# Optimization experiments

Hardware: AMD Instinct MI355X
Metric: run time of the kernel (lower is better)

Reference implementation:

```python
import jax, jax.numpy as jnp
import numpy as np

B, C, H, W = 16, 64, 64, 64
K = 512  # n_embeddings


def setup_inputs() -> dict:
    key = jax.random.key(0)
    k1, k2 = jax.random.split(key)
    inputs = jax.random.normal(k1, (B, C, H, W), dtype=jnp.float32)
    emb_weight = jax.random.normal(k2, (K, C), dtype=jnp.float32)
    weight = jnp.ones((K,), dtype=jnp.float32)  # EMA cluster-size buffer
    return {"inputs": inputs, "emb_weight": emb_weight, "weight": weight}


def reference(inputs, emb_weight, weight):
    sg = jax.lax.stop_gradient
    # BCHW -> BHWC
    x = jnp.transpose(inputs, (0, 2, 3, 1))  # [B,H,W,C]
    flat = x.reshape(-1, x.shape[-1])        # [N,C]
    n = flat.shape[0]
    k = emb_weight.shape[0]
    # squared euclidean distances [N,K] (argmin identical to cdist argmin)
    d = (
        jnp.sum(flat * flat, axis=-1, keepdims=True)
        - 2.0 * (flat @ emb_weight.T)
        + jnp.sum(emb_weight * emb_weight, axis=-1)
    )
    indices = jnp.argmin(d, axis=1)  # [N]
    # avg_probs = mean over rows of one-hot mask == normalized histogram
    avg_probs = jnp.bincount(indices, length=k).astype(jnp.float32) / jnp.float32(n)
    perplexity = jnp.exp(-jnp.sum(avg_probs * jnp.log(avg_probs + 1e-10)))
    # straight-through quantization
    q = emb_weight[indices].reshape(x.shape)  # [B,H,W,C]
    quantized = sg(q) + x - sg(x)
    commitment_loss = jnp.mean((sg(quantized) - x) ** 2)
    active_codes = jnp.sum(weight >= 0.01)
    out = jnp.transpose(quantized, (0, 3, 1, 2))  # back to BCHW
    return out, commitment_loss, perplexity, active_codes, indices
```

## Files before the change

kernel.cpp:

```cpp
#include <hip/hip_runtime.h>

#define HW 4096
#define CHW 262144
#define OUT_ELEMS 4194304
#define FLT_BIG 3.4e38f

typedef __attribute__((ext_vector_type(8))) short  short8;
typedef __attribute__((ext_vector_type(4))) float  floatx4;
typedef __attribute__((ext_vector_type(4))) int    intx4;


__device__ __forceinline__ unsigned bf16_rne(float f) {
    unsigned u = __float_as_uint(f);
    return (u + 0x7FFFu + ((u >> 16) & 1u)) >> 16;
}

__device__ __forceinline__ void split8(const float* f, intx4* hi, intx4* lo) {
    unsigned h[4], l[4];
#pragma unroll
    for (int j = 0; j < 4; ++j) {
        const unsigned h0 = bf16_rne(f[2 * j]);
        const unsigned h1 = bf16_rne(f[2 * j + 1]);
        const float hf0 = __uint_as_float(h0 << 16);
        const float hf1 = __uint_as_float(h1 << 16);
        const unsigned l0 = bf16_rne(f[2 * j] - hf0);
        const unsigned l1 = bf16_rne(f[2 * j + 1] - hf1);
        h[j] = h0 | (h1 << 16);
        l[j] = l0 | (l1 << 16);
    }
    *hi = intx4{(int)h[0], (int)h[1], (int)h[2], (int)h[3]};
    *lo = intx4{(int)l[0], (int)l[1], (int)l[2], (int)l[3]};
}

__global__ void vq_prep(const float* __restrict__ emb,
                        unsigned short* __restrict__ pfrag,
                        float* __restrict__ enorm) {
    const int t = threadIdx.x;
    const int lane = t & 63;
    const int code = (blockIdx.x << 2) + (t >> 6);
    const int c = lane;
    const float v = emb[(code << 6) + c];
    const unsigned hb = bf16_rne(v);
    const float hf    = __uint_as_float(hb << 16);
    const unsigned lb = bf16_rne(v - hf);
    const int nc = code >> 6, grp = (code & 63) >> 4, n = code & 15;
    const int q = (c & 31) >> 3, o = c & 7;
    const int jh = c >> 5;
    const int jl = 2 + (c >> 5);
    pfrag[((((size_t)(nc*4 + jh)*4 + grp)*4 + q)*16 + n)*8 + o] = (unsigned short)hb;
    pfrag[((((size_t)(nc*4 + jl)*4 + grp)*4 + q)*16 + n)*8 + o] = (unsigned short)lb;
    float s = v * v;
#pragma unroll
    for (int off = 32; off > 0; off >>= 1) s += __shfl_xor(s, off, 64);
    if (lane == 0) enorm[code] = -0.5f * s;
}

__global__ __launch_bounds__(256)
void vq_main(const float* __restrict__ x_in, const float* __restrict__ emb,
             const unsigned short* __restrict__ pfrag,
             const float* __restrict__ enorm,
             float* __restrict__ out, float* __restrict__ idx_out,
             double* __restrict__ ws_sse) {
    __shared__ float  b1s[2][64], b2s[2][64];
    __shared__ int    i1s[2][64], i2s[2][64];
    __shared__ int    c1i[64], c2i[64];
    __shared__ double parts[4][65];
    __shared__ double ls_red[4];

    const int t     = threadIdx.x;
    const int lane  = t & 63;
    const int wv    = t >> 6;
    const int col   = lane & 15;
    const int quad  = lane >> 4;
    const int blk   = blockIdx.x;
    const int khalf = wv & 1;
    const int mset  = wv >> 1;
    const int ncol0 = khalf << 5;
    const int b = blk >> 6, h = blk & 63;
    const float* xb = x_in + (size_t)b * CHW + h * 64;

    short8 Xh[2][2], Xl[2][2];
#pragma unroll
    for (int T = 0; T < 2; ++T) {
        const int row = (mset << 5) + (T << 4) + col;
#pragma unroll
        for (int u = 0; u < 2; ++u) {
            float f[8];
#pragma unroll
            for (int j = 0; j < 8; ++j) {
                const int c = (u << 5) + (quad << 3) + j;
                f[j] = xb[(size_t)c * HW + row];
            }
            intx4 hi, lo;
            split8(f, &hi, &lo);
            Xh[T][u] = __builtin_bit_cast(short8, hi);
            Xl[T][u] = __builtin_bit_cast(short8, lo);
        }
    }

    float B1a[2], B2a[2], B1b[2], B2b[2];
    int   I1a[2], I2a[2], I1b[2], I2b[2];
#pragma unroll
    for (int T = 0; T < 2; ++T) {
        B1a[T] = -FLT_BIG; B2a[T] = -FLT_BIG; B1b[T] = -FLT_BIG; B2b[T] = -FLT_BIG;
        I1a[T] = 0x3FFFFFFF; I2a[T] = 0x3FFFFFFF; I1b[T] = 0x3FFFFFFF; I2b[T] = 0x3FFFFFFF;
    }

    const char*  pf  = (const char*)pfrag + (size_t)lane * 16 + ((size_t)khalf << 11);
    const float* enp = enorm + ncol0 + (quad << 2);

#pragma unroll 2
    for (int nc = 0; nc < 8; ++nc) {
        const char* base = pf + ((size_t)nc << 14);
        const int K0 = nc << 6;
        const floatx4 e0v = *(const floatx4*)(enp + K0);
        const floatx4 e1v = *(const floatx4*)(enp + K0 + 16);
        floatx4 a0[2] = {{0.f,0.f,0.f,0.f},{0.f,0.f,0.f,0.f}};
        floatx4 a1[2] = {{0.f,0.f,0.f,0.f},{0.f,0.f,0.f,0.f}};
#define BLD(j, g) (*(const short8*)(base + ((j) << 12) + ((g) << 10)))
        {
            const short8 e0 = BLD(0, 0), e1 = BLD(0, 1);
#pragma unroll
            for (int T = 0; T < 2; ++T) {
                a0[T] = __builtin_amdgcn_mfma_f32_16x16x32_bf16(e0, Xh[T][0], a0[T], 0, 0, 0);
                a1[T] = __builtin_amdgcn_mfma_f32_16x16x32_bf16(e1, Xh[T][0], a1[T], 0, 0, 0);
                a0[T] = __builtin_amdgcn_mfma_f32_16x16x32_bf16(e0, Xl[T][0], a0[T], 0, 0, 0);
                a1[T] = __builtin_amdgcn_mfma_f32_16x16x32_bf16(e1, Xl[T][0], a1[T], 0, 0, 0);
            }
        }
        {
            const short8 e0 = BLD(1, 0), e1 = BLD(1, 1);
#pragma unroll
            for (int T = 0; T < 2; ++T) {
                a0[T] = __builtin_amdgcn_mfma_f32_16x16x32_bf16(e0, Xh[T][1], a0[T], 0, 0, 0);
                a1[T] = __builtin_amdgcn_mfma_f32_16x16x32_bf16(e1, Xh[T][1], a1[T], 0, 0, 0);
                a0[T] = __builtin_amdgcn_mfma_f32_16x16x32_bf16(e0, Xl[T][1], a0[T], 0, 0, 0);
                a1[T] = __builtin_amdgcn_mfma_f32_16x16x32_bf16(e1, Xl[T][1], a1[T], 0, 0, 0);
            }
        }
        {
            const short8 e0 = BLD(2, 0), e1 = BLD(2, 1);
#pragma unroll
            for (int T = 0; T < 2; ++T) {
                a0[T] = __builtin_amdgcn_mfma_f32_16x16x32_bf16(e0, Xh[T][0], a0[T], 0, 0, 0);
                a1[T] = __builtin_amdgcn_mfma_f32_16x16x32_bf16(e1, Xh[T][0], a1[T], 0, 0, 0);
            }
        }
        {
            const short8 e0 = BLD(3, 0), e1 = BLD(3, 1);
#pragma unroll
            for (int T = 0; T < 2; ++T) {
                a0[T] = __builtin_amdgcn_mfma_f32_16x16x32_bf16(e0, Xh[T][1], a0[T], 0, 0, 0);
                a1[T] = __builtin_amdgcn_mfma_f32_16x16x32_bf16(e1, Xh[T][1], a1[T], 0, 0, 0);
            }
        }
#undef BLD

        const int cb = K0 + ncol0 + (quad << 2);
#pragma unroll
        for (int T = 0; T < 2; ++T) {
#pragma unroll
            for (int reg = 0; reg < 4; ++reg) {
                const float da = a0[T][reg] + e0v[reg];
                if (da > B1a[T])      { B2a[T] = B1a[T]; I2a[T] = I1a[T]; B1a[T] = da; I1a[T] = cb + reg; }
                else if (da > B2a[T]) { B2a[T] = da; I2a[T] = cb + reg; }
                const float db = a1[T][reg] + e1v[reg];
                if (db > B1b[T])      { B2b[T] = B1b[T]; I2b[T] = I1b[T]; B1b[T] = db; I1b[T] = cb + 16 + reg; }
                else if (db > B2b[T]) { B2b[T] = db; I2b[T] = cb + 16 + reg; }
            }
        }
    }

#pragma unroll
    for (int T = 0; T < 2; ++T) {
        float B1, B2; int I1, I2;
        if (B1b[T] > B1a[T] || (B1b[T] == B1a[T] && I1b[T] < I1a[T])) {
            B1 = B1b[T]; I1 = I1b[T];
            if (B1a[T] > B2b[T] || (B1a[T] == B2b[T] && I1a[T] < I2b[T])) { B2 = B1a[T]; I2 = I1a[T]; }
            else                                                          { B2 = B2b[T]; I2 = I2b[T]; }
        } else {
            B1 = B1a[T]; I1 = I1a[T];
            if (B1b[T] > B2a[T] || (B1b[T] == B2a[T] && I1b[T] < I2a[T])) { B2 = B1b[T]; I2 = I1b[T]; }
            else                                                          { B2 = B2a[T]; I2 = I2a[T]; }
        }
#pragma unroll
        for (int off = 16; off <= 32; off <<= 1) {
            const float ob1 = __shfl_xor(B1, off, 64);
            const int   oi1 = __shfl_xor(I1, off, 64);
            const float ob2 = __shfl_xor(B2, off, 64);
            const int   oi2 = __shfl_xor(I2, off, 64);
            if (ob1 > B1 || (ob1 == B1 && oi1 < I1)) {
                float nb2; int ni2;
                if (B1 > ob2 || (B1 == ob2 && I1 < oi2)) { nb2 = B1; ni2 = I1; }
                else                                     { nb2 = ob2; ni2 = oi2; }
                B1 = ob1; I1 = oi1; B2 = nb2; I2 = ni2;
            } else if (ob1 > B2 || (ob1 == B2 && oi1 < I2)) {
                B2 = ob1; I2 = oi1;
            }
        }
        if (lane < 16) {
            const int row = (mset << 5) + (T << 4) + lane;
            b1s[khalf][row] = B1; b2s[khalf][row] = B2;
            i1s[khalf][row] = I1; i2s[khalf][row] = I2;
        }
    }
    __syncthreads();

    if (t < 64) {
        const int r = t;
        float b1 = b1s[0][r], b2 = b2s[0][r];
        int   i1 = i1s[0][r], i2 = i2s[0][r];
        const float c1 = b1s[1][r]; const int j1 = i1s[1][r];
        const float c2 = b2s[1][r]; const int j2 = i2s[1][r];
        if (c1 > b1 || (c1 == b1 && j1 < i1))      { b2 = b1; i2 = i1; b1 = c1; i1 = j1; }
        else if (c1 > b2 || (c1 == b2 && j1 < i2)) { b2 = c1; i2 = j1; }
        if (c2 > b2 || (c2 == b2 && j2 < i2))      { b2 = c2; i2 = j2; }
        c1i[r] = i1; c2i[r] = i2;
    }
    __syncthreads();

    const int r = t & 63;
    const int k = t >> 6;
    {
        const int ch = k >> 1;
        const int code = (k & 1) ? c2i[r] : c1i[r];
        const float* ep = emb + ((size_t)code << 6) + (ch << 5);
        const float* xq = xb + r;
        double d0 = 0.0, d1 = 0.0;
#pragma unroll
        for (int cc = 0; cc < 32; cc += 2) {
            const int c = (ch << 5) + cc;
            const double f0 = (double)xq[(size_t)c * HW]       - (double)ep[cc];
            const double f1 = (double)xq[(size_t)(c + 1) * HW] - (double)ep[cc + 1];
            d0 = fma(f0, f0, d0);
            d1 = fma(f1, f1, d1);
        }
        parts[k][r] = d0 + d1;
    }
    __syncthreads();

    int win;
    {
        const double d1 = parts[0][r] + parts[2][r];
        const double d2 = parts[1][r] + parts[3][r];
        win = c1i[r];
        const int i2 = c2i[r];
        if (d2 < d1 || (d2 == d1 && i2 < win)) win = i2;
        if (t < 64) idx_out[(blk << 6) + r] = (float)win;
    }

    {
        const int c0 = k << 4;
        const float* xp = xb + r;
        float*       op = out + (size_t)b * CHW + h * 64 + r;
        const float* eq = emb + ((size_t)win << 6);
        float sse_local = 0.f;
#pragma unroll
        for (int cc = 0; cc < 16; ++cc) {
            const int c = c0 + cc;
            const float qc = eq[c];
            const float dx = qc - xp[(size_t)c * HW];
            sse_local = fmaf(dx, dx, sse_local);
            op[(size_t)c * HW] = qc;
        }
#pragma unroll
        for (int off = 32; off > 0; off >>= 1)
            sse_local += __shfl_down(sse_local, off, 64);
        if (lane == 0) ls_red[wv] = (double)sse_local;
        __syncthreads();
        if (t == 0)
            ws_sse[blk] = (ls_red[0] + ls_red[1]) + (ls_red[2] + ls_red[3]);
    }
}

__global__ void vq_hist(const float* __restrict__ idx_out,
                        unsigned* __restrict__ part) {
    __shared__ unsigned hs[512];
    const int t = threadIdx.x;
    hs[t] = 0u; hs[t + 256] = 0u;
    __syncthreads();
    const float4* ip = (const float4*)(idx_out + (blockIdx.x << 12));
#pragma unroll
    for (int i = 0; i < 4; ++i) {
        const float4 v = ip[(i << 8) + t];
        atomicAdd(&hs[(int)v.x], 1u);
        atomicAdd(&hs[(int)v.y], 1u);
        atomicAdd(&hs[(int)v.z], 1u);
        atomicAdd(&hs[(int)v.w], 1u);
    }
    __syncthreads();
    unsigned* pp = part + (blockIdx.x << 9);
    pp[t] = hs[t]; pp[t + 256] = hs[t + 256];
}

__global__ void vq_scal(const unsigned* __restrict__ part,
                        const double* __restrict__ ws_sse,
                        const float* __restrict__ weight,
                        float* __restrict__ scal) {
    __shared__ double redt[8], reds[8];
    __shared__ int    redi[8];
    const int k = threadIdx.x;
    const int lane = k & 63, wv = k >> 6;
    unsigned cnt = 0;
#pragma unroll
    for (int p = 0; p < 16; ++p) cnt += part[(p << 9) + k];
    const double pr = (double)cnt / 65536.0;
    double term = pr * log(pr + 1e-10);
    double ssep = 0.0;
#pragma unroll
    for (int j = 0; j < 2; ++j) ssep += ws_sse[k + (j << 9)];
    int act = (weight[k] >= 0.01f) ? 1 : 0;
#pragma unroll
    for (int off = 32; off > 0; off >>= 1) {
        term += __shfl_down(term, off, 64);
        ssep += __shfl_down(ssep, off, 64);
        act  += __shfl_down(act,  off, 64);
    }
    if (lane == 0) { redt[wv] = term; reds[wv] = ssep; redi[wv] = act; }
    __syncthreads();
    if (k == 0) {
        double s = 0.0, ss = 0.0; int a = 0;
#pragma unroll
        for (int i = 0; i < 8; ++i) { s += redt[i]; ss += reds[i]; a += redi[i]; }
        scal[0] = (float)(ss / 4194304.0);
        scal[1] = (float)exp(-s);
        scal[2] = (float)a;
    }
}

extern "C" void kernel_launch(void* const* d_in, const int* in_sizes, int n_in,
                              void* d_out, int out_size, void* d_ws, size_t ws_size,
                              hipStream_t stream) {
    const float* x      = (const float*)d_in[0];
    const float* emb    = (const float*)d_in[1];
    const float* weight = (const float*)d_in[2];

    float* out = (float*)d_out;
    float*          enorm  = (float*)d_ws;
    unsigned short* pfrag  = (unsigned short*)((char*)d_ws + 4096);
    double*         ws_sse = (double*)((char*)d_ws + 135168);
    unsigned*       part   = (unsigned*)((char*)d_ws + 151552);

    float* scal    = out + OUT_ELEMS;
    float* idx_out = out + OUT_ELEMS + 3;

    vq_prep<<<128, 256, 0, stream>>>(emb, pfrag, enorm);
    vq_main<<<1024, 256, 0, stream>>>(x, emb, pfrag, enorm, out, idx_out, ws_sse);
    vq_hist<<<16, 256, 0, stream>>>(idx_out, part);
    vq_scal<<<1, 512, 0, stream>>>(part, ws_sse, weight, scal);
}
```

Baseline: 104.9 us.

## Double-buffer codebook fragments in LDS and fuse histogram with scalar reduction

The main kernel now stages each 16 KB chunk of codebook fragments into a double-buffered LDS array. It prefetches the next chunk into registers while the MFMAs run on the current one, with a block barrier per chunk, instead of having every wave read fragments straight from global memory. The separate histogram and scalar kernels are merged into one, using global atomics and a last-block-done counter (reset in the prep kernel), which removes one launch. The cost is 32 KB of LDS per block, which can lower occupancy, plus a barrier on every chunk iteration.

```diff
diff --git a/kernel.cpp b/kernel.cpp
--- a/kernel.cpp
+++ b/kernel.cpp
@@ -34,9 +34,15 @@
 
 __global__ void vq_prep(const float* __restrict__ emb,
                         unsigned short* __restrict__ pfrag,
-                        float* __restrict__ enorm) {
+                        float* __restrict__ enorm,
+                        unsigned* __restrict__ hist,
+                        unsigned* __restrict__ done) {
     const int t = threadIdx.x;
     const int lane = t & 63;
+    if (blockIdx.x == 0) {
+        hist[t] = 0u; hist[t + 256] = 0u;
+        if (t == 0) *done = 0u;
+    }
     const int code = (blockIdx.x << 2) + (t >> 6);
     const int c = lane;
     const float v = emb[(code << 6) + c];
@@ -61,6 +67,7 @@
              const float* __restrict__ enorm,
              float* __restrict__ out, float* __restrict__ idx_out,
              double* __restrict__ ws_sse) {
+    __shared__ unsigned short cbuf[2][8192];
     __shared__ float  b1s[2][64], b2s[2][64];
     __shared__ int    i1s[2][64], i2s[2][64];
     __shared__ int    c1i[64], c2i[64];
@@ -79,6 +86,11 @@
     const int b = blk >> 6, h = blk & 63;
     const float* xb = x_in + (size_t)b * CHW + h * 64;
 
+    intx4 s0[4];
+#pragma unroll
+    for (int i = 0; i < 4; ++i)
+        s0[i] = *(const intx4*)((const char*)pfrag + (i << 12) + (t << 4));
+
     short8 Xh[2][2], Xl[2][2];
 #pragma unroll
     for (int T = 0; T < 2; ++T) {
@@ -98,6 +110,11 @@
         }
     }
 
+#pragma unroll
+    for (int i = 0; i < 4; ++i)
+        *(intx4*)((char*)&cbuf[0][0] + (i << 12) + (t << 4)) = s0[i];
+    __syncthreads();
+
     float B1a[2], B2a[2], B1b[2], B2b[2];
     int   I1a[2], I2a[2], I1b[2], I2b[2];
 #pragma unroll
@@ -106,17 +123,25 @@
         I1a[T] = 0x3FFFFFFF; I2a[T] = 0x3FFFFFFF; I1b[T] = 0x3FFFFFFF; I2b[T] = 0x3FFFFFFF;
     }
 
-    const char*  pf  = (const char*)pfrag + (size_t)lane * 16 + ((size_t)khalf << 11);
     const float* enp = enorm + ncol0 + (quad << 2);
+    const int lbo = (khalf << 11) + (lane << 4);
 
 #pragma unroll 2
     for (int nc = 0; nc < 8; ++nc) {
-        const char* base = pf + ((size_t)nc << 14);
+        const int cur = nc & 1;
+        intx4 st[4];
+        if (nc < 7) {
+#pragma unroll
+            for (int i = 0; i < 4; ++i)
+                st[i] = *(const intx4*)((const char*)pfrag +
+                          ((size_t)(nc + 1) << 14) + (i << 12) + (t << 4));
+        }
         const int K0 = nc << 6;
         const floatx4 e0v = *(const floatx4*)(enp + K0);
         const floatx4 e1v = *(const floatx4*)(enp + K0 + 16);
         floatx4 a0[2] = {{0.f,0.f,0.f,0.f},{0.f,0.f,0.f,0.f}};
         floatx4 a1[2] = {{0.f,0.f,0.f,0.f},{0.f,0.f,0.f,0.f}};
+        const char* base = (const char*)&cbuf[cur][0] + lbo;
 #define BLD(j, g) (*(const short8*)(base + ((j) << 12) + ((g) << 10)))
         {
             const short8 e0 = BLD(0, 0), e1 = BLD(0, 1);
@@ -169,6 +194,13 @@
                 else if (db > B2b[T]) { B2b[T] = db; I2b[T] = cb + 16 + reg; }
             }
         }
+
+        if (nc < 7) {
+#pragma unroll
+            for (int i = 0; i < 4; ++i)
+                *(intx4*)((char*)&cbuf[cur ^ 1][0] + (i << 12) + (t << 4)) = st[i];
+        }
+        __syncthreads();
     }
 
 #pragma unroll
@@ -273,10 +305,17 @@
     }
 }
 
-__global__ void vq_hist(const float* __restrict__ idx_out,
-                        unsigned* __restrict__ part) {
+__global__ void vq_hist2(const float* __restrict__ idx_out,
+                         const double* __restrict__ ws_sse,
+                         const float* __restrict__ weight,
+                         unsigned* __restrict__ hist,
+                         unsigned* __restrict__ done,
+                         float* __restrict__ scal) {
     __shared__ unsigned hs[512];
+    __shared__ double redt[4], reds[4];
+    __shared__ int    redi[4], lastf;
     const int t = threadIdx.x;
+    const int lane = t & 63, wv = t >> 6;
     hs[t] = 0u; hs[t + 256] = 0u;
     __syncthreads();
     const float4* ip = (const float4*)(idx_out + (blockIdx.x << 12));
@@ -289,42 +328,44 @@
         atomicAdd(&hs[(int)v.w], 1u);
     }
     __syncthreads();
-    unsigned* pp = part + (blockIdx.x << 9);
-    pp[t] = hs[t]; pp[t + 256] = hs[t + 256];
-}
-
-__global__ void vq_scal(const unsigned* __restrict__ part,
-                        const double* __restrict__ ws_sse,
-                        const float* __restrict__ weight,
-                        float* __restrict__ scal) {
-    __shared__ double redt[8], reds[8];
-    __shared__ int    redi[8];
-    const int k = threadIdx.x;
-    const int lane = k & 63, wv = k >> 6;
-    unsigned cnt = 0;
-#pragma unroll
-    for (int p = 0; p < 16; ++p) cnt += part[(p << 9) + k];
-    const double pr = (double)cnt / 65536.0;
-    double term = pr * log(pr + 1e-10);
-    double ssep = 0.0;
-#pragma unroll
-    for (int j = 0; j < 2; ++j) ssep += ws_sse[k + (j << 9)];
-    int act = (weight[k] >= 0.01f) ? 1 : 0;
-#pragma unroll
-    for (int off = 32; off > 0; off >>= 1) {
-        term += __shfl_down(term, off, 64);
-        ssep += __shfl_down(ssep, off, 64);
-        act  += __shfl_down(act,  off, 64);
-    }
-    if (lane == 0) { redt[wv] = term; reds[wv] = ssep; redi[wv] = act; }
-    __syncthreads();
-    if (k == 0) {
-        double s = 0.0, ss = 0.0; int a = 0;
-#pragma unroll
-        for (int i = 0; i < 8; ++i) { s += redt[i]; ss += reds[i]; a += redi[i]; }
-        scal[0] = (float)(ss / 4194304.0);
-        scal[1] = (float)exp(-s);
-        scal[2] = (float)a;
+    if (hs[t])       atomicAdd(&hist[t],       hs[t]);
+    if (hs[t + 256]) atomicAdd(&hist[t + 256], hs[t + 256]);
+    __syncthreads();
+
+    if (t == 0) {
+        lastf = (__hip_atomic_fetch_add(done, 1u, __ATOMIC_RELAXED,
+                                        __HIP_MEMORY_SCOPE_AGENT) == 15u) ? 1 : 0;
+    }
+    __syncthreads();
+    if (lastf) {
+        double term = 0.0, ssep = 0.0; int act = 0;
+#pragma unroll
+        for (int j = 0; j < 2; ++j) {
+            const int kk = t + (j << 8);
+            const unsigned cnt =
+                __hip_atomic_load(&hist[kk], __ATOMIC_RELAXED, __HIP_MEMORY_SCOPE_AGENT);
+            const double pr = (double)cnt * (1.0 / 65536.0);
+            term += pr * log(pr + 1e-10);
+            act  += (weight[kk] >= 0.01f) ? 1 : 0;
+        }
+#pragma unroll
+        for (int j = 0; j < 4; ++j) ssep += ws_sse[t + (j << 8)];
+#pragma unroll
+        for (int off = 32; off > 0; off >>= 1) {
+            term += __shfl_down(term, off, 64);
+            ssep += __shfl_down(ssep, off, 64);
+            act  += __shfl_down(act,  off, 64);
+        }
+        if (lane == 0) { redt[wv] = term; reds[wv] = ssep; redi[wv] = act; }
+        __syncthreads();
+        if (t == 0) {
+            const double s  = (redt[0] + redt[1]) + (redt[2] + redt[3]);
+            const double ss = (reds[0] + reds[1]) + (reds[2] + reds[3]);
+            const int    a  = redi[0] + redi[1] + redi[2] + redi[3];
+            scal[0] = (float)(ss * (1.0 / 4194304.0));
+            scal[1] = (float)exp(-s);
+            scal[2] = (float)a;
+        }
     }
 }
 
@@ -339,13 +380,13 @@
     float*          enorm  = (float*)d_ws;
     unsigned short* pfrag  = (unsigned short*)((char*)d_ws + 4096);
     double*         ws_sse = (double*)((char*)d_ws + 135168);
-    unsigned*       part   = (unsigned*)((char*)d_ws + 151552);
+    unsigned*       hist   = (unsigned*)((char*)d_ws + 143360);
+    unsigned*       done   = (unsigned*)((char*)d_ws + 145408);
 
     float* scal    = out + OUT_ELEMS;
     float* idx_out = out + OUT_ELEMS + 3;
 
-    vq_prep<<<128, 256, 0, stream>>>(emb, pfrag, enorm);
+    vq_prep<<<128, 256, 0, stream>>>(emb, pfrag, enorm, hist, done);
     vq_main<<<1024, 256, 0, stream>>>(x, emb, pfrag, enorm, out, idx_out, ws_sse);
-    vq_hist<<<16, 256, 0, stream>>>(idx_out, part);
-    vq_scal<<<1, 512, 0, stream>>>(part, ws_sse, weight, scal);
-}
+    vq_hist2<<<16, 256, 0, stream>>>(idx_out, ws_sse, weight, hist, done, scal);
+}
```

New measurement: 102.6 us. 1.02x faster.
